# Kernel tuning notes

Measured on AMD Instinct MI355X. Metric: run time of the kernel, lower is better.

## Reference

```python
import jax, jax.numpy as jnp
import numpy as np
import math

B, S, E, H = 4, 2048, 1024, 16

def setup_inputs() -> dict:
    key = jax.random.key(0)
    k1, k2, k3 = jax.random.split(key, 3)
    scale_in = 1.0 / math.sqrt(E)
    x = jax.random.normal(k1, (B, S, E), dtype=jnp.float32)
    W_attn = jax.random.normal(k2, (E, 3 * E), dtype=jnp.float32) * scale_in
    b_attn = jnp.zeros((3 * E,), dtype=jnp.float32)
    W_proj = jax.random.normal(k3, (E, E), dtype=jnp.float32) * scale_in
    b_proj = jnp.zeros((E,), dtype=jnp.float32)
    return {"x": x, "W_attn": W_attn, "b_attn": b_attn, "W_proj": W_proj, "b_proj": b_proj}

def reference(x, W_attn, b_attn, W_proj, b_proj):
    batch, seq, emb = x.shape
    hd = emb // H  # head_dim
    qkv = x @ W_attn + b_attn                      # [B,S,3E]
    q, k, v = jnp.split(qkv, 3, axis=-1)
    # [B,S,E] -> [B,H,S,hd]
    q = q.reshape(batch, seq, H, hd).transpose(0, 2, 1, 3)
    k = k.reshape(batch, seq, H, hd).transpose(0, 2, 1, 3)
    v = v.reshape(batch, seq, H, hd).transpose(0, 2, 1, 3)
    scores = jnp.einsum('bhqd,bhkd->bhqk', q, k) * (1.0 / math.sqrt(hd))
    causal = jnp.tril(jnp.ones((seq, seq), dtype=bool))
    scores = jnp.where(causal[None, None, :, :], scores, jnp.finfo(scores.dtype).min)
    attn = jax.nn.softmax(scores, axis=-1)         # dropout p=0 -> identity
    out = jnp.einsum('bhqk,bhkd->bhqd', attn, v)   # [B,H,S,hd]
    out = out.transpose(0, 2, 1, 3).reshape(batch, seq, emb)
    return out @ W_proj + b_proj
```

## Files before the change

### kernel.cpp

```cpp
#include <hip/hip_runtime.h>

typedef __bf16 bf16;
typedef __bf16 bf16x8_t __attribute__((ext_vector_type(8)));
typedef __bf16 bf16x4_t __attribute__((ext_vector_type(4)));
typedef float f32x4_t __attribute__((ext_vector_type(4)));

#define S_ 2048
#define E_ 1024
#define HD 64
#define LOG2E 1.4426950408889634f
#define QSCALE (0.125f * LOG2E)

__device__ __forceinline__ void gl_lds16(const bf16* g, bf16* l) {
  __builtin_amdgcn_global_load_lds(
      (const __attribute__((address_space(1))) unsigned int*)g,
      (__attribute__((address_space(3))) unsigned int*)l, 16, 0, 0);
}

__global__ void cvt4(const float* __restrict__ in, bf16* __restrict__ out) {
  int i = (blockIdx.x * 256 + threadIdx.x) * 4;
  float4 v = *(const float4*)(in + i);
  bf16x4_t o = { (bf16)v.x, (bf16)v.y, (bf16)v.z, (bf16)v.w };
  *(bf16x4_t*)(out + i) = o;
}

__global__ void transpose_cvt(const float* __restrict__ in, bf16* __restrict__ out,
                              int R, int C) {
  __shared__ float tile[32][33];
  int c0 = blockIdx.x * 32, r0 = blockIdx.y * 32;
  int tx = threadIdx.x & 31, ty = threadIdx.x >> 5;
#pragma unroll
  for (int i = 0; i < 32; i += 8)
    tile[ty + i][tx] = in[(size_t)(r0 + ty + i) * C + c0 + tx];
  __syncthreads();
#pragma unroll
  for (int i = 0; i < 32; i += 8)
    out[(size_t)(c0 + ty + i) * R + r0 + tx] = (bf16)tile[tx][ty + i];
}

template <int MODE>
__global__ __launch_bounds__(256, 2)
void gemm128(const bf16* __restrict__ A, const bf16* __restrict__ Bt,
             const float* __restrict__ bias,
             bf16* __restrict__ Q, bf16* __restrict__ K, bf16* __restrict__ Vt,
             float* __restrict__ Out) {
  __shared__ __align__(16) bf16 As[128 * 64];
  __shared__ __align__(16) bf16 Bs[128 * 64];
  const int tid = threadIdx.x;
  const int wave = tid >> 6, lane = tid & 63;
  const int quad = lane >> 4, l16 = lane & 15;
  const int wm = wave >> 1, wn = wave & 1;
  const int bm = blockIdx.x, bn = blockIdx.y;

  f32x4_t acc[4][4];
#pragma unroll
  for (int i = 0; i < 4; i++)
#pragma unroll
    for (int j = 0; j < 4; j++) acc[i][j] = (f32x4_t){0.f, 0.f, 0.f, 0.f};

  for (int k0 = 0; k0 < 1024; k0 += 64) {
    __syncthreads();
#pragma unroll
    for (int it = 0; it < 4; it++) {
      int id = it * 256 + tid;
      int row = id >> 3, c = id & 7;
      int sc = (c ^ (row & 7)) * 8;
      gl_lds16(A + (size_t)(bm * 128 + row) * 1024 + k0 + sc, As + id * 8);
      gl_lds16(Bt + (size_t)(bn * 128 + row) * 1024 + k0 + sc, Bs + id * 8);
    }
    __syncthreads();
#pragma unroll
    for (int ks = 0; ks < 2; ks++) {
      bf16x8_t af[4], bfr[4];
#pragma unroll
      for (int i = 0; i < 4; i++) {
        int row = wm * 64 + i * 16 + l16;
        af[i] = *(const bf16x8_t*)&As[row * 64 + (((ks * 4 + quad) ^ (row & 7)) * 8)];
      }
#pragma unroll
      for (int j = 0; j < 4; j++) {
        int row = wn * 64 + j * 16 + l16;
        bfr[j] = *(const bf16x8_t*)&Bs[row * 64 + (((ks * 4 + quad) ^ (row & 7)) * 8)];
      }
#pragma unroll
      for (int i = 0; i < 4; i++)
#pragma unroll
        for (int j = 0; j < 4; j++)
          acc[i][j] = __builtin_amdgcn_mfma_f32_16x16x32_bf16(af[i], bfr[j], acc[i][j], 0, 0, 0);
    }
  }

  if (MODE == 0) {
#pragma unroll
    for (int j = 0; j < 4; j++) {
      int n_g = bn * 128 + wn * 64 + j * 16 + l16;
      float bv = bias[n_g];
      int which = n_g >> 10;
      int cc = n_g & 1023;
      int hh = cc >> 6, dd = cc & 63;
#pragma unroll
      for (int i = 0; i < 4; i++) {
        int m0 = bm * 128 + wm * 64 + i * 16 + quad * 4;
        int bb = m0 >> 11, ss0 = m0 & 2047;
        int bhn = bb * 16 + hh;
        if (which == 2) {
          bf16x4_t pk;
#pragma unroll
          for (int r = 0; r < 4; r++) pk[r] = (bf16)(acc[i][j][r] + bv);
          *(bf16x4_t*)&Vt[((size_t)bhn * 64 + dd) * 2048 + ss0] = pk;
        } else {
          bf16* dst = (which == 0) ? Q : K;
          float scl = (which == 0) ? QSCALE : 1.f;
#pragma unroll
          for (int r = 0; r < 4; r++)
            dst[((size_t)bhn * 2048 + ss0 + r) * 64 + dd] = (bf16)((acc[i][j][r] + bv) * scl);
        }
      }
    }
  } else {
#pragma unroll
    for (int j = 0; j < 4; j++) {
      int n_g = bn * 128 + wn * 64 + j * 16 + l16;
      float bv = bias[n_g];
#pragma unroll
      for (int i = 0; i < 4; i++) {
        int m0 = bm * 128 + wm * 64 + i * 16 + quad * 4;
#pragma unroll
        for (int r = 0; r < 4; r++)
          Out[(size_t)(m0 + r) * 1024 + n_g] = acc[i][j][r] + bv;
      }
    }
  }
}

__global__ __launch_bounds__(256, 2)
void attn_kernel(const bf16* __restrict__ Q, const bf16* __restrict__ K,
                 const bf16* __restrict__ Vt, bf16* __restrict__ O) {
  extern __shared__ __align__(16) bf16 smem[];
  bf16* Ks = smem;
  bf16* Vs = smem + 16384;
  bf16* Ps = smem + 32768;
  const int tid = threadIdx.x;
  const int wave = tid >> 6, lane = tid & 63;
  const int quad = lane >> 4, l16 = lane & 15;
  const int pid = blockIdx.x, bh = blockIdx.y;
  const int b = bh >> 4, h = bh & 15;

  const bf16* Qg = Q + (size_t)bh * S_ * HD;
  const bf16* Kg = K + (size_t)bh * S_ * HD;
  const bf16* Vg = Vt + (size_t)bh * HD * S_;
  bf16* Pw = Ps + wave * 2048;

  auto stage = [&](int c, int kb) {
    const bf16* Ksrc = Kg + (size_t)kb * 128 * HD;
    const bf16* Vsrc = Vg + kb * 128;
    bf16* Kd = Ks + c * 8192;
    bf16* Vd = Vs + c * 8192;
#pragma unroll
    for (int it = 0; it < 4; it++) {
      int id = it * 256 + tid;
      {
        int row = id >> 3, cc = id & 7;
        gl_lds16(Ksrc + row * 64 + ((cc ^ (row & 7)) * 8), Kd + id * 8);
      }
      {
        int d = id >> 4, cc = id & 15;
        gl_lds16(Vsrc + (size_t)d * S_ + ((cc ^ (d & 7)) * 8), Vd + id * 8);
      }
    }
  };

  int cur = 0;
  stage(0, 0);

  for (int qi = 0; qi < 2; qi++) {
    const int qb = qi ? (15 - pid) : pid;
    bf16x8_t qf[2][2];
#pragma unroll
    for (int ni = 0; ni < 2; ni++)
#pragma unroll
      for (int ks = 0; ks < 2; ks++)
        qf[ni][ks] = *(const bf16x8_t*)(Qg +
            (size_t)(qb * 128 + wave * 32 + ni * 16 + l16) * HD + ks * 32 + quad * 8);

    f32x4_t o[4][2];
#pragma unroll
    for (int mi = 0; mi < 4; mi++)
#pragma unroll
      for (int ni = 0; ni < 2; ni++) o[mi][ni] = (f32x4_t){0.f, 0.f, 0.f, 0.f};
    float m_[2] = {-1e30f, -1e30f}, l_[2] = {0.f, 0.f};

    if (qi == 0) __syncthreads();

    for (int kb = 0; kb <= qb; kb++) {
      if (kb < qb) stage(cur ^ 1, kb + 1);
      else if (qi == 0) stage(cur ^ 1, 0);

      const bf16* Kc = Ks + cur * 8192;
      const bf16* Vc = Vs + cur * 8192;

      f32x4_t sacc[8][2];
#pragma unroll
      for (int mi = 0; mi < 8; mi++)
#pragma unroll
        for (int ni = 0; ni < 2; ni++) sacc[mi][ni] = (f32x4_t){0.f, 0.f, 0.f, 0.f};
#pragma unroll
      for (int ks = 0; ks < 2; ks++)
#pragma unroll
        for (int mi = 0; mi < 8; mi++) {
          int kr = mi * 16 + l16;
          bf16x8_t kf = *(const bf16x8_t*)&Kc[kr * 64 + (((ks * 4 + quad) ^ (kr & 7)) * 8)];
          sacc[mi][0] = __builtin_amdgcn_mfma_f32_16x16x32_bf16(kf, qf[0][ks], sacc[mi][0], 0, 0, 0);
          sacc[mi][1] = __builtin_amdgcn_mfma_f32_16x16x32_bf16(kf, qf[1][ks], sacc[mi][1], 0, 0, 0);
        }

      if (kb == qb) {
#pragma unroll
        for (int mi = 0; mi < 8; mi++)
#pragma unroll
          for (int ni = 0; ni < 2; ni++) {
            int qrow = wave * 32 + ni * 16 + l16;
            int krow = mi * 16 + quad * 4;
#pragma unroll
            for (int r = 0; r < 4; r++)
              if (krow + r > qrow) sacc[mi][ni][r] = -1e30f;
          }
      }

#pragma unroll
      for (int ni = 0; ni < 2; ni++) {
        float mx = sacc[0][ni][0];
#pragma unroll
        for (int mi = 0; mi < 8; mi++)
#pragma unroll
          for (int r = 0; r < 4; r++) mx = fmaxf(mx, sacc[mi][ni][r]);
        mx = fmaxf(mx, __shfl_xor(mx, 16));
        mx = fmaxf(mx, __shfl_xor(mx, 32));
        float mnew = fmaxf(m_[ni], mx);
        float alpha = __builtin_amdgcn_exp2f(m_[ni] - mnew);
        m_[ni] = mnew;
        float rs = 0.f;
#pragma unroll
        for (int mi = 0; mi < 8; mi++)
#pragma unroll
          for (int r = 0; r < 4; r++) {
            float p = __builtin_amdgcn_exp2f(sacc[mi][ni][r] - mnew);
            sacc[mi][ni][r] = p;
            rs += p;
          }
        rs += __shfl_xor(rs, 16);
        rs += __shfl_xor(rs, 32);
        l_[ni] = alpha * l_[ni] + rs;
#pragma unroll
        for (int mi = 0; mi < 4; mi++)
#pragma unroll
          for (int r = 0; r < 4; r++) o[mi][ni][r] *= alpha;
      }

#pragma unroll
      for (int hh = 0; hh < 2; hh++) {
#pragma unroll
        for (int ni = 0; ni < 2; ni++) {
          int qr = ni * 16 + l16;
#pragma unroll
          for (int mm = 0; mm < 4; mm++) {
            bf16x4_t pk;
#pragma unroll
            for (int r = 0; r < 4; r++) pk[r] = (bf16)sacc[hh * 4 + mm][ni][r];
            int c = mm * 2 + (quad >> 1);
            *(bf16x4_t*)&Pw[qr * 64 + ((c ^ (qr & 7)) * 8) + (quad & 1) * 4] = pk;
          }
        }
#pragma unroll
        for (int k2 = 0; k2 < 2; k2++) {
          int ks2 = hh * 2 + k2;
          bf16x8_t vb[4], pa[2];
#pragma unroll
          for (int mi = 0; mi < 4; mi++) {
            int d = mi * 16 + l16;
            vb[mi] = *(const bf16x8_t*)&Vc[d * 128 + (((ks2 * 4 + quad) ^ (d & 7)) * 8)];
          }
#pragma unroll
          for (int ni = 0; ni < 2; ni++) {
            int qr = ni * 16 + l16;
            pa[ni] = *(const bf16x8_t*)&Pw[qr * 64 + (((k2 * 4 + quad) ^ (qr & 7)) * 8)];
          }
#pragma unroll
          for (int mi = 0; mi < 4; mi++)
#pragma unroll
            for (int ni = 0; ni < 2; ni++)
              o[mi][ni] = __builtin_amdgcn_mfma_f32_16x16x32_bf16(vb[mi], pa[ni], o[mi][ni], 0, 0, 0);
        }
      }

      __syncthreads();
      cur ^= 1;
    }

#pragma unroll
    for (int ni = 0; ni < 2; ni++) {
      float inv = 1.0f / l_[ni];
      int q_g = qb * 128 + wave * 32 + ni * 16 + l16;
      size_t rowb = (size_t)(b * S_ + q_g) * E_ + h * HD;
#pragma unroll
      for (int mi = 0; mi < 4; mi++) {
        bf16x4_t ov;
#pragma unroll
        for (int r = 0; r < 4; r++) ov[r] = (bf16)(o[mi][ni][r] * inv);
        *(bf16x4_t*)&O[rowb + mi * 16 + quad * 4] = ov;
      }
    }
  }
}

extern "C" void kernel_launch(void* const* d_in, const int* in_sizes, int n_in,
                              void* d_out, int out_size, void* d_ws, size_t ws_size,
                              hipStream_t stream) {
  const float* x      = (const float*)d_in[0];
  const float* W_attn = (const float*)d_in[1];
  const float* b_attn = (const float*)d_in[2];
  const float* W_proj = (const float*)d_in[3];
  const float* b_proj = (const float*)d_in[4];
  float* out = (float*)d_out;

  bf16* xb  = (bf16*)d_ws;
  bf16* Wat = xb + 8388608ull;
  bf16* Wpt = Wat + 3145728ull;
  bf16* Qb  = Wpt + 1048576ull;
  bf16* Kb  = Qb + 8388608ull;
  bf16* Vtb = Kb + 8388608ull;
  bf16* AOb = xb;

  cvt4<<<8192, 256, 0, stream>>>(x, xb);
  transpose_cvt<<<dim3(96, 32), 256, 0, stream>>>(W_attn, Wat, 1024, 3072);
  transpose_cvt<<<dim3(32, 32), 256, 0, stream>>>(W_proj, Wpt, 1024, 1024);
  gemm128<0><<<dim3(64, 24), 256, 0, stream>>>(xb, Wat, b_attn, Qb, Kb, Vtb, nullptr);
  attn_kernel<<<dim3(8, 64), 256, 81920, stream>>>(Qb, Kb, Vtb, AOb);
  gemm128<1><<<dim3(64, 8), 256, 0, stream>>>(AOb, Wpt, b_proj, nullptr, nullptr, nullptr, out);
}
```

Before: 248.1 us.

## Defer online-softmax rescaling, tree-reduce max, hoist V loads, raise MFMA priority

The attention softmax now skips updating the running max, and skips rescaling the output accumulator, whenever every lane's new block max stays within a threshold of the current reference max. The max reduction becomes a vectorised tree and the row-sum uses two vector accumulators. V fragments for both k-steps are loaded before P is written to LDS, and the MFMA sections are wrapped in s_setprio so matrix work is favoured across waves. This trims per-block exp, multiply and dependency-chain cost, but adds a wave-uniform branch, holds more V fragments in registers, and lets exponent values reach up to 2^8 before rescaling.

Result: no change. 246.9 us (-0.5%).

```diff
diff --git a/kernel.cpp b/kernel.cpp
--- a/kernel.cpp
+++ b/kernel.cpp
@@ -10,11 +10,19 @@
 #define HD 64
 #define LOG2E 1.4426950408889634f
 #define QSCALE (0.125f * LOG2E)
+#define DEFER_THR 8.0f
 
 __device__ __forceinline__ void gl_lds16(const bf16* g, bf16* l) {
   __builtin_amdgcn_global_load_lds(
       (const __attribute__((address_space(1))) unsigned int*)g,
       (__attribute__((address_space(3))) unsigned int*)l, 16, 0, 0);
+}
+
+__device__ __forceinline__ f32x4_t vmax4(f32x4_t a, f32x4_t b) {
+  f32x4_t r;
+  r[0] = fmaxf(a[0], b[0]); r[1] = fmaxf(a[1], b[1]);
+  r[2] = fmaxf(a[2], b[2]); r[3] = fmaxf(a[3], b[3]);
+  return r;
 }
 
 __global__ void cvt4(const float* __restrict__ in, bf16* __restrict__ out) {
@@ -204,6 +212,7 @@
       for (int mi = 0; mi < 8; mi++)
 #pragma unroll
         for (int ni = 0; ni < 2; ni++) sacc[mi][ni] = (f32x4_t){0.f, 0.f, 0.f, 0.f};
+      __builtin_amdgcn_s_setprio(1);
 #pragma unroll
       for (int ks = 0; ks < 2; ks++)
 #pragma unroll
@@ -213,6 +222,7 @@
           sacc[mi][0] = __builtin_amdgcn_mfma_f32_16x16x32_bf16(kf, qf[0][ks], sacc[mi][0], 0, 0, 0);
           sacc[mi][1] = __builtin_amdgcn_mfma_f32_16x16x32_bf16(kf, qf[1][ks], sacc[mi][1], 0, 0, 0);
         }
+      __builtin_amdgcn_s_setprio(0);
 
       if (kb == qb) {
 #pragma unroll
@@ -229,36 +239,71 @@
 
 #pragma unroll
       for (int ni = 0; ni < 2; ni++) {
-        float mx = sacc[0][ni][0];
-#pragma unroll
-        for (int mi = 0; mi < 8; mi++)
-#pragma unroll
-          for (int r = 0; r < 4; r++) mx = fmaxf(mx, sacc[mi][ni][r]);
+        f32x4_t t0 = vmax4(sacc[0][ni], sacc[1][ni]);
+        f32x4_t t1 = vmax4(sacc[2][ni], sacc[3][ni]);
+        f32x4_t t2 = vmax4(sacc[4][ni], sacc[5][ni]);
+        f32x4_t t3 = vmax4(sacc[6][ni], sacc[7][ni]);
+        t0 = vmax4(t0, t1); t2 = vmax4(t2, t3); t0 = vmax4(t0, t2);
+        float mx = fmaxf(fmaxf(t0[0], t0[1]), fmaxf(t0[2], t0[3]));
         mx = fmaxf(mx, __shfl_xor(mx, 16));
         mx = fmaxf(mx, __shfl_xor(mx, 32));
-        float mnew = fmaxf(m_[ni], mx);
-        float alpha = __builtin_amdgcn_exp2f(m_[ni] - mnew);
-        m_[ni] = mnew;
-        float rs = 0.f;
-#pragma unroll
-        for (int mi = 0; mi < 8; mi++)
-#pragma unroll
-          for (int r = 0; r < 4; r++) {
-            float p = __builtin_amdgcn_exp2f(sacc[mi][ni][r] - mnew);
-            sacc[mi][ni][r] = p;
-            rs += p;
-          }
-        rs += __shfl_xor(rs, 16);
-        rs += __shfl_xor(rs, 32);
-        l_[ni] = alpha * l_[ni] + rs;
-#pragma unroll
-        for (int mi = 0; mi < 4; mi++)
-#pragma unroll
-          for (int r = 0; r < 4; r++) o[mi][ni][r] *= alpha;
+        float mref = m_[ni];
+        if (__all(mx <= mref + DEFER_THR)) {
+          f32x4_t a0 = {0.f, 0.f, 0.f, 0.f}, a1 = {0.f, 0.f, 0.f, 0.f};
+#pragma unroll
+          for (int mi = 0; mi < 4; mi++) {
+#pragma unroll
+            for (int r = 0; r < 4; r++) {
+              sacc[mi][ni][r] = __builtin_amdgcn_exp2f(sacc[mi][ni][r] - mref);
+              sacc[mi + 4][ni][r] = __builtin_amdgcn_exp2f(sacc[mi + 4][ni][r] - mref);
+            }
+            a0 += sacc[mi][ni];
+            a1 += sacc[mi + 4][ni];
+          }
+          a0 += a1;
+          float rs = (a0[0] + a0[1]) + (a0[2] + a0[3]);
+          rs += __shfl_xor(rs, 16);
+          rs += __shfl_xor(rs, 32);
+          l_[ni] += rs;
+        } else {
+          float mnew = fmaxf(mref, mx);
+          float alpha = __builtin_amdgcn_exp2f(mref - mnew);
+          m_[ni] = mnew;
+          f32x4_t a0 = {0.f, 0.f, 0.f, 0.f}, a1 = {0.f, 0.f, 0.f, 0.f};
+#pragma unroll
+          for (int mi = 0; mi < 4; mi++) {
+#pragma unroll
+            for (int r = 0; r < 4; r++) {
+              sacc[mi][ni][r] = __builtin_amdgcn_exp2f(sacc[mi][ni][r] - mnew);
+              sacc[mi + 4][ni][r] = __builtin_amdgcn_exp2f(sacc[mi + 4][ni][r] - mnew);
+            }
+            a0 += sacc[mi][ni];
+            a1 += sacc[mi + 4][ni];
+          }
+          a0 += a1;
+          float rs = (a0[0] + a0[1]) + (a0[2] + a0[3]);
+          rs += __shfl_xor(rs, 16);
+          rs += __shfl_xor(rs, 32);
+          l_[ni] = alpha * l_[ni] + rs;
+#pragma unroll
+          for (int mi = 0; mi < 4; mi++)
+#pragma unroll
+            for (int r = 0; r < 4; r++) o[mi][ni][r] *= alpha;
+        }
       }
 
 #pragma unroll
       for (int hh = 0; hh < 2; hh++) {
+        bf16x8_t vb[2][4];
+#pragma unroll
+        for (int k2 = 0; k2 < 2; k2++) {
+          int ks2 = hh * 2 + k2;
+#pragma unroll
+          for (int mi = 0; mi < 4; mi++) {
+            int d = mi * 16 + l16;
+            vb[k2][mi] = *(const bf16x8_t*)&Vc[d * 128 + (((ks2 * 4 + quad) ^ (d & 7)) * 8)];
+          }
+        }
 #pragma unroll
         for (int ni = 0; ni < 2; ni++) {
           int qr = ni * 16 + l16;
@@ -273,23 +318,19 @@
         }
 #pragma unroll
         for (int k2 = 0; k2 < 2; k2++) {
-          int ks2 = hh * 2 + k2;
-          bf16x8_t vb[4], pa[2];
-#pragma unroll
-          for (int mi = 0; mi < 4; mi++) {
-            int d = mi * 16 + l16;
-            vb[mi] = *(const bf16x8_t*)&Vc[d * 128 + (((ks2 * 4 + quad) ^ (d & 7)) * 8)];
-          }
+          bf16x8_t pa[2];
 #pragma unroll
           for (int ni = 0; ni < 2; ni++) {
             int qr = ni * 16 + l16;
             pa[ni] = *(const bf16x8_t*)&Pw[qr * 64 + (((k2 * 4 + quad) ^ (qr & 7)) * 8)];
           }
+          __builtin_amdgcn_s_setprio(1);
 #pragma unroll
           for (int mi = 0; mi < 4; mi++)
 #pragma unroll
             for (int ni = 0; ni < 2; ni++)
-              o[mi][ni] = __builtin_amdgcn_mfma_f32_16x16x32_bf16(vb[mi], pa[ni], o[mi][ni], 0, 0, 0);
+              o[mi][ni] = __builtin_amdgcn_mfma_f32_16x16x32_bf16(vb[k2][mi], pa[ni], o[mi][ni], 0, 0, 0);
+          __builtin_amdgcn_s_setprio(0);
         }
       }
 
```
